# Performance work log

Hardware: AMD Instinct MI355X
Metric: run time of the kernel (lower is better)

## Reference

```python
import jax, jax.numpy as jnp
import numpy as np

NUM_EMBEDDINGS = 1024
EMBEDDING_DIM = 256
COMMITMENT_COST = 0.25


def setup_inputs() -> dict:
    key = jax.random.key(0)
    k1, k2 = jax.random.split(key)
    inputs = jax.random.normal(k1, (32, EMBEDDING_DIM, 32, 32), dtype=jnp.float32)
    # codebook init matches torch: uniform(-1/K, 1/K)
    weight = jax.random.uniform(
        k2, (NUM_EMBEDDINGS, EMBEDDING_DIM), dtype=jnp.float32,
        minval=-1.0 / NUM_EMBEDDINGS, maxval=1.0 / NUM_EMBEDDINGS)
    return {"inputs": inputs, "weight": weight}


def reference(inputs, weight):
    # inputs: [B, C, H, W] with C == EMBEDDING_DIM; weight: [K, D]
    x = jnp.transpose(inputs, (0, 2, 3, 1))            # [B, H, W, D]
    input_shape = x.shape
    flat = x.reshape(-1, EMBEDDING_DIM)                # [N, D]

    distances = (jnp.sum(flat * flat, axis=1, keepdims=True)
                 + jnp.sum(weight * weight, axis=1)
                 - 2.0 * (flat @ weight.T))
    encoding_indices = jnp.argmin(distances, axis=1)   # [N]
    encodings = jax.nn.one_hot(encoding_indices, NUM_EMBEDDINGS, dtype=jnp.float32)  # [N, K]

    # one_hot @ weight == gather; use gather for efficiency (same values)
    quantized = weight[encoding_indices].reshape(input_shape)  # [B, H, W, D]

    e_latent_loss = jnp.mean((jax.lax.stop_gradient(quantized) - x) ** 2)
    q_latent_loss = jnp.mean((quantized - jax.lax.stop_gradient(x)) ** 2)
    loss = q_latent_loss + COMMITMENT_COST * e_latent_loss

    # straight-through estimator
    quantized_st = x + jax.lax.stop_gradient(quantized - x)

    avg_probs = jnp.mean(encodings, axis=0)            # [K]
    perplexity = jnp.exp(-jnp.sum(avg_probs * jnp.log(avg_probs + 1e-10)))

    return (loss,
            jnp.transpose(quantized_st, (0, 3, 1, 2)),  # back to [B, C, H, W]
            perplexity,
            encodings)
```

## Files before the change

kernel.cpp:

```cpp
#include <hip/hip_runtime.h>
#include <hip/hip_bf16.h>

#define HWDIM 1024
#define DDIM 256
#define KCODES 1024
#define NROWS 32768
#define BSTRIDE (DDIM * HWDIM)
#define GUARD 1.5e-4f

typedef __attribute__((ext_vector_type(8))) short short8;
typedef __attribute__((ext_vector_type(4))) float f32x4;
typedef unsigned long long ull;


__device__ __forceinline__ unsigned short f2bf(float v) {
  __hip_bfloat16 b = __float2bfloat16(v);
  return *reinterpret_cast<unsigned short*>(&b);
}
__device__ __forceinline__ float bf2f(unsigned short u) {
  __hip_bfloat16 b;
  *reinterpret_cast<unsigned short*>(&b) = u;
  return __bfloat162float(b);
}
__device__ __forceinline__ ull pk(float d, int k) {
  unsigned ub = __float_as_uint(d);
  ub = (ub & 0x80000000u) ? ~ub : (ub | 0x80000000u);
  return ((ull)ub << 32) | (unsigned)k;
}
__device__ __forceinline__ float keyq(ull key) {
  unsigned ub = (unsigned)(key >> 32);
  unsigned orig = (ub & 0x80000000u) ? (ub & 0x7FFFFFFFu) : ~ub;
  return __uint_as_float(orig);
}

__device__ __forceinline__ float pair128_sq(const float* p, int stride) {
  float a[8];
#pragma unroll
  for (int j = 0; j < 8; ++j) { float v = p[j * stride]; a[j] = __fmul_rn(v, v); }
  for (int i = 8; i < 128; i += 8) {
#pragma unroll
    for (int j = 0; j < 8; ++j) {
      float v = p[(i + j) * stride];
      a[j] = __fadd_rn(a[j], __fmul_rn(v, v));
    }
  }
  float s01 = __fadd_rn(a[0], a[1]), s23 = __fadd_rn(a[2], a[3]);
  float s45 = __fadd_rn(a[4], a[5]), s67 = __fadd_rn(a[6], a[7]);
  return __fadd_rn(__fadd_rn(s01, s23), __fadd_rn(s45, s67));
}

__global__ __launch_bounds__(256) void k_prep(
    const float* __restrict__ w, float* __restrict__ wT, float* __restrict__ ss,
    int* __restrict__ hist, double* __restrict__ loss,
    int* __restrict__ wcount, int* __restrict__ pcount,
    unsigned short* __restrict__ wh8, unsigned short* __restrict__ wl8) {
  __shared__ float tile[64][65];
  const int t = threadIdx.x;
  int g = blockIdx.x * 256 + t;
  {
    int k = g >> 5, oct = g & 31;
    const float* p = w + k * DDIM + oct * 8;
    short8 hv, lv;
#pragma unroll
    for (int j = 0; j < 8; ++j) {
      float v = p[j];
      unsigned short h = f2bf(v);
      unsigned short l = f2bf(__fsub_rn(v, bf2f(h)));
      hv[j] = (short)h; lv[j] = (short)l;
    }
    *(short8*)&wh8[oct * 8192 + k * 8] = hv;
    *(short8*)&wl8[oct * 8192 + k * 8] = lv;
  }
  if (g < KCODES) {
    hist[g] = 0;
    const float* p = w + g * DDIM;
    ss[g] = __fadd_rn(pair128_sq(p, 1), pair128_sq(p + 128, 1));
  }
  if (g == 0) { *loss = 0.0; *wcount = 0; *pcount = 0; }
  if (blockIdx.x < 64) {
    const int k0 = (blockIdx.x & 15) * 64, d0 = (blockIdx.x >> 4) * 64;
    const int c = t & 63, r = t >> 6;
#pragma unroll
    for (int m = 0; m < 16; ++m)
      tile[r + m * 4][c] = w[(k0 + r + m * 4) * DDIM + d0 + c];
    __syncthreads();
#pragma unroll
    for (int m = 0; m < 16; ++m)
      wT[(size_t)(d0 + r + m * 4) * KCODES + k0 + c] = tile[c][r + m * 4];
  }
}

__global__ __launch_bounds__(256) void k_argmfma(
    const float* __restrict__ in,
    const unsigned short* __restrict__ wh8, const unsigned short* __restrict__ wl8,
    const float* __restrict__ ss, unsigned* __restrict__ kkarr,
    int* __restrict__ wlist, int* __restrict__ wcount,
    int* __restrict__ plist, int* __restrict__ pcount) {
  __shared__ __align__(16) unsigned short Ah[32 * 32 * 8];
  __shared__ __align__(16) unsigned short Al[32 * 32 * 8];
  __shared__ __align__(16) float ss_l[1024];
  __shared__ ull best1[32], best2[32], best3[32];

  const int t = threadIdx.x;
  const int n0 = blockIdx.x * 32;
  const int b = n0 >> 10, hw0 = n0 & 1023;

  const int wv = t >> 6, ln = t & 63;
  const int cw = wv * 64;
  const int l15 = ln & 15, quad = ln >> 4;

  {
    const int hw = t & 31, dg = t >> 5;
    const float* xp = in + b * BSTRIDE + hw0 + hw;
#pragma unroll
    for (int dd = 0; dd < 32; dd += 2) {
      int d = dg * 32 + dd;
      float f0 = xp[d * HWDIM], f1 = xp[(d + 1) * HWDIM];
      unsigned short h0 = f2bf(f0);
      unsigned short l0 = f2bf(__fsub_rn(f0, bf2f(h0)));
      unsigned short h1 = f2bf(f1);
      unsigned short l1 = f2bf(__fsub_rn(f1, bf2f(h1)));
      int base = ((d >> 3) * 32 + hw) * 8 + (d & 7);
      *(unsigned*)&Ah[base] = (unsigned)h0 | ((unsigned)h1 << 16);
      *(unsigned*)&Al[base] = (unsigned)l0 | ((unsigned)l1 << 16);
    }
  }
  *(float4*)&ss_l[t * 4] = *(const float4*)&ss[t * 4];
  if (t < 32) { best1[t] = ~0ull; best2[t] = ~0ull; best3[t] = ~0ull; }
  __syncthreads();

  ull rb1[8], rb2[8], rb3[8];
#pragma unroll
  for (int i = 0; i < 8; ++i) { rb1[i] = ~0ull; rb2[i] = ~0ull; rb3[i] = ~0ull; }

  for (int kb = 0; kb < 4; ++kb) {
    const int cb = kb * 256 + cw;
    f32x4 acc[2][4];
#pragma unroll
    for (int rt = 0; rt < 2; ++rt)
#pragma unroll
      for (int ct = 0; ct < 4; ++ct) acc[rt][ct] = (f32x4){0.f, 0.f, 0.f, 0.f};

#pragma unroll
    for (int ki = 0; ki < 8; ++ki) {
      const int obase = ki * 4 + quad;
      short8 ah[2], al[2], bh[4], bl[4];
#pragma unroll
      for (int rt = 0; rt < 2; ++rt) {
        int row = rt * 16 + l15;
        ah[rt] = *(const short8*)&Ah[(obase * 32 + row) * 8];
        al[rt] = *(const short8*)&Al[(obase * 32 + row) * 8];
      }
#pragma unroll
      for (int ct = 0; ct < 4; ++ct) {
        int off = obase * 8192 + (cb + ct * 16 + l15) * 8;
        bh[ct] = *(const short8*)&wh8[off];
        bl[ct] = *(const short8*)&wl8[off];
      }
      __builtin_amdgcn_s_setprio(1);
#pragma unroll
      for (int rt = 0; rt < 2; ++rt)
#pragma unroll
        for (int ct = 0; ct < 4; ++ct) {
          acc[rt][ct] = __builtin_amdgcn_mfma_f32_16x16x32_bf16(ah[rt], bh[ct], acc[rt][ct], 0, 0, 0);
          acc[rt][ct] = __builtin_amdgcn_mfma_f32_16x16x32_bf16(ah[rt], bl[ct], acc[rt][ct], 0, 0, 0);
          acc[rt][ct] = __builtin_amdgcn_mfma_f32_16x16x32_bf16(al[rt], bh[ct], acc[rt][ct], 0, 0, 0);
        }
      __builtin_amdgcn_s_setprio(0);
    }

    float sv[4];
#pragma unroll
    for (int ct = 0; ct < 4; ++ct) sv[ct] = ss_l[cb + ct * 16 + l15];
#pragma unroll
    for (int rt = 0; rt < 2; ++rt)
#pragma unroll
      for (int reg = 0; reg < 4; ++reg) {
        int idx = rt * 4 + reg;
        ull b1 = rb1[idx], b2 = rb2[idx], b3 = rb3[idx];
#pragma unroll
        for (int ct = 0; ct < 4; ++ct) {
          float q = fmaf(-2.f, acc[rt][ct][reg], sv[ct]);
          ull key = pk(q, cb + ct * 16 + l15);
          if (key < b1)      { b3 = b2; b2 = b1; b1 = key; }
          else if (key < b2) { b3 = b2; b2 = key; }
          else if (key < b3) { b3 = key; }
        }
        rb1[idx] = b1; rb2[idx] = b2; rb3[idx] = b3;
      }
  }

#pragma unroll
  for (int rt = 0; rt < 2; ++rt)
#pragma unroll
    for (int reg = 0; reg < 4; ++reg)
      atomicMin(&best1[rt * 16 + quad * 4 + reg], rb1[rt * 4 + reg]);
  __syncthreads();
#pragma unroll
  for (int rt = 0; rt < 2; ++rt)
#pragma unroll
    for (int reg = 0; reg < 4; ++reg) {
      int row = rt * 16 + quad * 4 + reg;
      int idx = rt * 4 + reg;
      ull sub = (rb1[idx] == best1[row]) ? rb2[idx] : rb1[idx];
      atomicMin(&best2[row], sub);
    }
  __syncthreads();
#pragma unroll
  for (int rt = 0; rt < 2; ++rt)
#pragma unroll
    for (int reg = 0; reg < 4; ++reg) {
      int row = rt * 16 + quad * 4 + reg;
      int idx = rt * 4 + reg;
      ull b1 = best1[row], b2 = best2[row];
      ull c = (rb1[idx] != b1 && rb1[idx] != b2) ? rb1[idx]
            : ((rb2[idx] != b1 && rb2[idx] != b2) ? rb2[idx] : rb3[idx]);
      atomicMin(&best3[row], c);
    }
  __syncthreads();
  if (t < 32) {
    ull k1 = best1[t];
    kkarr[n0 + t] = (unsigned)(k1 & 0xFFFFFFFFull);
    float q1 = keyq(k1);
    if (!(keyq(best2[t]) - q1 > GUARD)) {
      if (keyq(best3[t]) - q1 > GUARD) {
        int p = atomicAdd(pcount, 1);
        plist[p] = (n0 + t) | ((int)(best2[t] & 0xFFFFFFFFull) << 16);
      } else {
        int p = atomicAdd(wcount, 1);
        wlist[p] = n0 + t;
      }
    }
  }
}

__global__ __launch_bounds__(256) void k_fallback(
    const float* __restrict__ in, const float* __restrict__ w,
    const float* __restrict__ wT, const float* __restrict__ ss,
    const int* __restrict__ wlist, const int* __restrict__ wcount,
    const int* __restrict__ plist, const int* __restrict__ pcount,
    unsigned* __restrict__ kkarr) {
  __shared__ float xrow[256];
  __shared__ float rsh;
  __shared__ ull bmin;
  __shared__ ull pkeys[2];
  const int t = threadIdx.x;

  const int pc = *pcount;
  for (int i = blockIdx.x; i < pc; i += gridDim.x) {
    const int pe = plist[i];
    const int n = pe & 0xFFFF;
    const unsigned k2 = ((unsigned)pe) >> 16;
    const unsigned k1 = kkarr[n];
    const int b = n >> 10, hw = n & 1023;
    xrow[t] = in[b * BSTRIDE + t * HWDIM + hw];
    __syncthreads();
    if (t == 0) rsh = __fadd_rn(pair128_sq(xrow, 1), pair128_sq(xrow + 128, 1));
    __syncthreads();
    if (t < 2) {
      unsigned k = t ? k2 : k1;
      const float* wr = w + (size_t)k * DDIM;
      float m = 0.f;
      for (int d = 0; d < 256; ++d) m = fmaf(xrow[d], wr[d], m);
      float dist = fmaf(-2.f, m, __fadd_rn(rsh, ss[k]));
      pkeys[t] = pk(dist, (int)k);
    }
    __syncthreads();
    if (t == 0) {
      ull kmin = pkeys[0] < pkeys[1] ? pkeys[0] : pkeys[1];
      kkarr[n] = (unsigned)(kmin & 0xFFFFFFFFull);
    }
    __syncthreads();
  }

  const int cnt = *wcount;
  for (int i = blockIdx.x; i < cnt; i += gridDim.x) {
    const int n = wlist[i];
    const int b = n >> 10, hw = n & 1023;
    xrow[t] = in[b * BSTRIDE + t * HWDIM + hw];
    if (t == 0) bmin = ~0ull;
    __syncthreads();
    if (t == 0) rsh = __fadd_rn(pair128_sq(xrow, 1), pair128_sq(xrow + 128, 1));
    __syncthreads();
    float m[4] = {0.f, 0.f, 0.f, 0.f};
    for (int d = 0; d < 256; ++d) {
      float xv = xrow[d];
      const float* wd = wT + (size_t)d * KCODES + t;
      m[0] = fmaf(xv, wd[0], m[0]);
      m[1] = fmaf(xv, wd[256], m[1]);
      m[2] = fmaf(xv, wd[512], m[2]);
      m[3] = fmaf(xv, wd[768], m[3]);
    }
    ull lb = ~0ull;
#pragma unroll
    for (int j = 0; j < 4; ++j) {
      int k = t + j * 256;
      float dist = fmaf(-2.f, m[j], __fadd_rn(rsh, ss[k]));
      ull key = pk(dist, k);
      if (key < lb) lb = key;
    }
    atomicMin(&bmin, lb);
    __syncthreads();
    if (t == 0) kkarr[n] = (unsigned)(bmin & 0xFFFFFFFFull);
    __syncthreads();
  }
}

__global__ __launch_bounds__(256) void k_quantenc(
    const float* __restrict__ in, const float* __restrict__ w,
    const unsigned* __restrict__ kkarr, int* __restrict__ hist,
    float* __restrict__ enc, float* __restrict__ outq, double* __restrict__ loss) {
  __shared__ float wrow[64][65];
  __shared__ unsigned kk[64];
  __shared__ double red[256];

  const int t = threadIdx.x;
  const int q = blockIdx.x & 3;
  const int n0 = (blockIdx.x >> 2) * 64;
  const int dc = q * 64;
  const int c0 = q * 256;
  const int b = n0 >> 10, hw0 = n0 & 1023;

  if (t < 64) kk[t] = kkarr[n0 + t];
  __syncthreads();

  if (q == 0 && t < 64) atomicAdd(&hist[kk[t]], 1);

#pragma unroll 4
  for (int m = 0; m < 32; ++m) {
    int u = m * 256 + t;
    int r = u >> 7, c2 = u & 127;
    int cbase = c0 + c2 * 2;
    unsigned kr = kk[r];
    float2 v;
    v.x = (cbase == (int)kr) ? 1.0f : 0.0f;
    v.y = (cbase + 1 == (int)kr) ? 1.0f : 0.0f;
    *(float2*)&enc[(size_t)(n0 + r) * 1024 + cbase] = v;
  }

#pragma unroll
  for (int m = 0; m < 16; ++m) {
    int u = t + m * 256;
    int r = u >> 6, dd = u & 63;
    wrow[r][dd] = w[kk[r] * DDIM + dc + dd];
  }
  __syncthreads();

  const float* inb = in + b * BSTRIDE + hw0;
  float* outb = outq + b * BSTRIDE + hw0;
  const int hwl = t & 63, dl = t >> 6;
  double lsum = 0.0;
#pragma unroll
  for (int dd = 0; dd < 64; dd += 4) {
    int d = dc + dd + dl;
    float x = inb[d * HWDIM + hwl];
    float wv = wrow[hwl][dd + dl];
    float diff = __fsub_rn(wv, x);
    outb[d * HWDIM + hwl] = __fadd_rn(x, diff);
    lsum += (double)diff * (double)diff;
  }
  red[t] = lsum;
  __syncthreads();
  for (int s = 128; s > 0; s >>= 1) {
    if (t < s) red[t] += red[t + s];
    __syncthreads();
  }
  if (t == 0) atomicAdd(loss, red[0]);
}

__global__ void k_final(const int* __restrict__ hist, const double* __restrict__ loss,
                        float* __restrict__ out) {
  __shared__ double red[256];
  int t = threadIdx.x;
  double s = 0.0;
  for (int i = t; i < KCODES; i += 256) {
    double p = (double)hist[i] * (1.0 / 32768.0);
    s += p * log(p + 1e-10);
  }
  red[t] = s;
  __syncthreads();
  for (int st = 128; st > 0; st >>= 1) {
    if (t < st) red[t] += red[t + st];
    __syncthreads();
  }
  if (t == 0) {
    out[8388609] = (float)exp(-red[0]);
    double m = *loss / 8388608.0;
    out[0] = (float)(1.25 * m);
  }
}

extern "C" void kernel_launch(void* const* d_in, const int* in_sizes, int n_in,
                              void* d_out, int out_size, void* d_ws, size_t ws_size,
                              hipStream_t stream) {
  const float* in = (const float*)d_in[0];
  const float* w  = (const float*)d_in[1];
  float* out = (float*)d_out;

  char* wsb = (char*)d_ws;
  float*    wT     = (float*)   (wsb + 0);
  float*    ssp    = (float*)   (wsb + 1048576);
  unsigned* kkarr  = (unsigned*)(wsb + 1052672);
  int*      wlist  = (int*)     (wsb + 1183744);
  int*      hist   = (int*)     (wsb + 1314816);
  int*      plist  = (int*)     (wsb + 1318912);
  double*   loss   = (double*)  (wsb + 1449984);
  int*      wcount = (int*)     (wsb + 1449992);
  int*      pcount = (int*)     (wsb + 1449996);

  char* ob = (char*)d_out + 33554448;
  unsigned short* wh8 = (unsigned short*)(ob + 0);
  unsigned short* wl8 = (unsigned short*)(ob + 524288);
  float* encp = out + 8388610;

  k_prep<<<dim3(128), dim3(256), 0, stream>>>(w, wT, ssp, hist, loss, wcount, pcount, wh8, wl8);
  k_argmfma<<<dim3(1024), dim3(256), 0, stream>>>(in, wh8, wl8, ssp, kkarr,
                                                  wlist, wcount, plist, pcount);
  k_fallback<<<dim3(1024), dim3(256), 0, stream>>>(in, w, wT, ssp, wlist, wcount,
                                                   plist, pcount, kkarr);
  k_quantenc<<<dim3(2048), dim3(256), 0, stream>>>(in, w, kkarr, hist, encp,
                                                   out + 1, loss);
  k_final<<<dim3(1), dim3(256), 0, stream>>>(hist, loss, out);
}
```

Before: 355.7 us.

## Double rows per block in argmin MFMA kernel and pad LDS layout

Each block of the argmin MFMA kernel now handles 64 input rows instead of 32, so every codebook fragment loaded from global memory feeds twice as many MFMAs and the grid halves to 512 blocks. The A-operand LDS layout gets a padded stride to reduce bank conflicts, input loads use nontemporal hints, and the third-best tracker is shrunk to a 32-bit distance key to save registers. Launch bounds of one block per CU with 16 accumulator tiles raise register pressure and may reduce occupancy or cause spills.

```diff
diff --git a/kernel.cpp b/kernel.cpp
--- a/kernel.cpp
+++ b/kernel.cpp
@@ -7,6 +7,7 @@
 #define NROWS 32768
 #define BSTRIDE (DDIM * HWDIM)
 #define GUARD 1.5e-4f
+#define APAD 520
 
 typedef __attribute__((ext_vector_type(8))) short short8;
 typedef __attribute__((ext_vector_type(4))) float f32x4;
@@ -29,6 +30,10 @@
 }
 __device__ __forceinline__ float keyq(ull key) {
   unsigned ub = (unsigned)(key >> 32);
+  unsigned orig = (ub & 0x80000000u) ? (ub & 0x7FFFFFFFu) : ~ub;
+  return __uint_as_float(orig);
+}
+__device__ __forceinline__ float keyq32(unsigned ub) {
   unsigned orig = (ub & 0x80000000u) ? (ub & 0x7FFFFFFFu) : ~ub;
   return __uint_as_float(orig);
 }
@@ -90,19 +95,20 @@
   }
 }
 
-__global__ __launch_bounds__(256) void k_argmfma(
+__global__ __launch_bounds__(256, 1) void k_argmfma(
     const float* __restrict__ in,
     const unsigned short* __restrict__ wh8, const unsigned short* __restrict__ wl8,
     const float* __restrict__ ss, unsigned* __restrict__ kkarr,
     int* __restrict__ wlist, int* __restrict__ wcount,
     int* __restrict__ plist, int* __restrict__ pcount) {
-  __shared__ __align__(16) unsigned short Ah[32 * 32 * 8];
-  __shared__ __align__(16) unsigned short Al[32 * 32 * 8];
+  __shared__ __align__(16) unsigned short Ah[32 * APAD];
+  __shared__ __align__(16) unsigned short Al[32 * APAD];
   __shared__ __align__(16) float ss_l[1024];
-  __shared__ ull best1[32], best2[32], best3[32];
+  __shared__ ull best1[64], best2[64];
+  __shared__ unsigned best3[64];
 
   const int t = threadIdx.x;
-  const int n0 = blockIdx.x * 32;
+  const int n0 = blockIdx.x * 64;
   const int b = n0 >> 10, hw0 = n0 & 1023;
 
   const int wv = t >> 6, ln = t & 63;
@@ -110,46 +116,48 @@
   const int l15 = ln & 15, quad = ln >> 4;
 
   {
-    const int hw = t & 31, dg = t >> 5;
+    const int hw = t & 63, dg = t >> 6;
     const float* xp = in + b * BSTRIDE + hw0 + hw;
 #pragma unroll
-    for (int dd = 0; dd < 32; dd += 2) {
-      int d = dg * 32 + dd;
-      float f0 = xp[d * HWDIM], f1 = xp[(d + 1) * HWDIM];
+    for (int dd = 0; dd < 64; dd += 2) {
+      int d = dg * 64 + dd;
+      float f0 = __builtin_nontemporal_load(&xp[d * HWDIM]);
+      float f1 = __builtin_nontemporal_load(&xp[(d + 1) * HWDIM]);
       unsigned short h0 = f2bf(f0);
       unsigned short l0 = f2bf(__fsub_rn(f0, bf2f(h0)));
       unsigned short h1 = f2bf(f1);
       unsigned short l1 = f2bf(__fsub_rn(f1, bf2f(h1)));
-      int base = ((d >> 3) * 32 + hw) * 8 + (d & 7);
+      int base = (d >> 3) * APAD + hw * 8 + (d & 7);
       *(unsigned*)&Ah[base] = (unsigned)h0 | ((unsigned)h1 << 16);
       *(unsigned*)&Al[base] = (unsigned)l0 | ((unsigned)l1 << 16);
     }
   }
   *(float4*)&ss_l[t * 4] = *(const float4*)&ss[t * 4];
-  if (t < 32) { best1[t] = ~0ull; best2[t] = ~0ull; best3[t] = ~0ull; }
-  __syncthreads();
-
-  ull rb1[8], rb2[8], rb3[8];
-#pragma unroll
-  for (int i = 0; i < 8; ++i) { rb1[i] = ~0ull; rb2[i] = ~0ull; rb3[i] = ~0ull; }
+  if (t < 64) { best1[t] = ~0ull; best2[t] = ~0ull; best3[t] = 0xFFFFFFFFu; }
+  __syncthreads();
+
+  ull rb1[16], rb2[16];
+  unsigned rb3[16];
+#pragma unroll
+  for (int i = 0; i < 16; ++i) { rb1[i] = ~0ull; rb2[i] = ~0ull; rb3[i] = 0xFFFFFFFFu; }
 
   for (int kb = 0; kb < 4; ++kb) {
     const int cb = kb * 256 + cw;
-    f32x4 acc[2][4];
-#pragma unroll
-    for (int rt = 0; rt < 2; ++rt)
+    f32x4 acc[4][4];
+#pragma unroll
+    for (int rt = 0; rt < 4; ++rt)
 #pragma unroll
       for (int ct = 0; ct < 4; ++ct) acc[rt][ct] = (f32x4){0.f, 0.f, 0.f, 0.f};
 
 #pragma unroll
     for (int ki = 0; ki < 8; ++ki) {
       const int obase = ki * 4 + quad;
-      short8 ah[2], al[2], bh[4], bl[4];
-#pragma unroll
-      for (int rt = 0; rt < 2; ++rt) {
+      short8 ah[4], al[4], bh[4], bl[4];
+#pragma unroll
+      for (int rt = 0; rt < 4; ++rt) {
         int row = rt * 16 + l15;
-        ah[rt] = *(const short8*)&Ah[(obase * 32 + row) * 8];
-        al[rt] = *(const short8*)&Al[(obase * 32 + row) * 8];
+        ah[rt] = *(const short8*)&Ah[obase * APAD + row * 8];
+        al[rt] = *(const short8*)&Al[obase * APAD + row * 8];
       }
 #pragma unroll
       for (int ct = 0; ct < 4; ++ct) {
@@ -159,7 +167,7 @@
       }
       __builtin_amdgcn_s_setprio(1);
 #pragma unroll
-      for (int rt = 0; rt < 2; ++rt)
+      for (int rt = 0; rt < 4; ++rt)
 #pragma unroll
         for (int ct = 0; ct < 4; ++ct) {
           acc[rt][ct] = __builtin_amdgcn_mfma_f32_16x16x32_bf16(ah[rt], bh[ct], acc[rt][ct], 0, 0, 0);
@@ -173,31 +181,33 @@
 #pragma unroll
     for (int ct = 0; ct < 4; ++ct) sv[ct] = ss_l[cb + ct * 16 + l15];
 #pragma unroll
-    for (int rt = 0; rt < 2; ++rt)
+    for (int rt = 0; rt < 4; ++rt)
 #pragma unroll
       for (int reg = 0; reg < 4; ++reg) {
         int idx = rt * 4 + reg;
-        ull b1 = rb1[idx], b2 = rb2[idx], b3 = rb3[idx];
+        ull b1 = rb1[idx], b2 = rb2[idx];
+        unsigned b3 = rb3[idx];
 #pragma unroll
         for (int ct = 0; ct < 4; ++ct) {
           float q = fmaf(-2.f, acc[rt][ct][reg], sv[ct]);
           ull key = pk(q, cb + ct * 16 + l15);
-          if (key < b1)      { b3 = b2; b2 = b1; b1 = key; }
-          else if (key < b2) { b3 = b2; b2 = key; }
-          else if (key < b3) { b3 = key; }
+          unsigned k32 = (unsigned)(key >> 32);
+          if (key < b1)      { b3 = (unsigned)(b2 >> 32); b2 = b1; b1 = key; }
+          else if (key < b2) { b3 = (unsigned)(b2 >> 32); b2 = key; }
+          else if (k32 < b3) { b3 = k32; }
         }
         rb1[idx] = b1; rb2[idx] = b2; rb3[idx] = b3;
       }
   }
 
 #pragma unroll
-  for (int rt = 0; rt < 2; ++rt)
+  for (int rt = 0; rt < 4; ++rt)
 #pragma unroll
     for (int reg = 0; reg < 4; ++reg)
       atomicMin(&best1[rt * 16 + quad * 4 + reg], rb1[rt * 4 + reg]);
   __syncthreads();
 #pragma unroll
-  for (int rt = 0; rt < 2; ++rt)
+  for (int rt = 0; rt < 4; ++rt)
 #pragma unroll
     for (int reg = 0; reg < 4; ++reg) {
       int row = rt * 16 + quad * 4 + reg;
@@ -207,23 +217,24 @@
     }
   __syncthreads();
 #pragma unroll
-  for (int rt = 0; rt < 2; ++rt)
+  for (int rt = 0; rt < 4; ++rt)
 #pragma unroll
     for (int reg = 0; reg < 4; ++reg) {
       int row = rt * 16 + quad * 4 + reg;
       int idx = rt * 4 + reg;
       ull b1 = best1[row], b2 = best2[row];
-      ull c = (rb1[idx] != b1 && rb1[idx] != b2) ? rb1[idx]
-            : ((rb2[idx] != b1 && rb2[idx] != b2) ? rb2[idx] : rb3[idx]);
+      unsigned c = (rb1[idx] != b1 && rb1[idx] != b2) ? (unsigned)(rb1[idx] >> 32)
+                 : ((rb2[idx] != b1 && rb2[idx] != b2) ? (unsigned)(rb2[idx] >> 32)
+                                                       : rb3[idx]);
       atomicMin(&best3[row], c);
     }
   __syncthreads();
-  if (t < 32) {
+  if (t < 64) {
     ull k1 = best1[t];
     kkarr[n0 + t] = (unsigned)(k1 & 0xFFFFFFFFull);
     float q1 = keyq(k1);
     if (!(keyq(best2[t]) - q1 > GUARD)) {
-      if (keyq(best3[t]) - q1 > GUARD) {
+      if (keyq32(best3[t]) - q1 > GUARD) {
         int p = atomicAdd(pcount, 1);
         plist[p] = (n0 + t) | ((int)(best2[t] & 0xFFFFFFFFull) << 16);
       } else {
@@ -414,8 +425,8 @@
   float* encp = out + 8388610;
 
   k_prep<<<dim3(128), dim3(256), 0, stream>>>(w, wT, ssp, hist, loss, wcount, pcount, wh8, wl8);
-  k_argmfma<<<dim3(1024), dim3(256), 0, stream>>>(in, wh8, wl8, ssp, kkarr,
-                                                  wlist, wcount, plist, pcount);
+  k_argmfma<<<dim3(512), dim3(256), 0, stream>>>(in, wh8, wl8, ssp, kkarr,
+                                                 wlist, wcount, plist, pcount);
   k_fallback<<<dim3(1024), dim3(256), 0, stream>>>(in, w, wT, ssp, wlist, wcount,
                                                    plist, pcount, kkarr);
   k_quantenc<<<dim3(2048), dim3(256), 0, stream>>>(in, w, kkarr, hist, encp,
```

Result: faster. 348.3 us (-2.1%).

## Shrink argmin kernel register footprint to raise occupancy in MFMA distance search

Applied to the files above, without the earlier changes.

Halves each wave's column tile (two 16-column tiles instead of four, eight codebook passes instead of four), stores the third-best candidate as a 32-bit value instead of a 64-bit key, and adds a launch_bounds occupancy hint of 4. The goal is to cut VGPR use so more waves fit per CU and hide codebook load latency. Input loads become nontemporal. In exchange each wave issues more loop iterations, with less reuse of A fragments per B load, and the third-best now keeps only the distance bits, which is enough for the guard test.

```diff
diff --git a/kernel.cpp b/kernel.cpp
--- a/kernel.cpp
+++ b/kernel.cpp
@@ -29,6 +29,10 @@
 }
 __device__ __forceinline__ float keyq(ull key) {
   unsigned ub = (unsigned)(key >> 32);
+  unsigned orig = (ub & 0x80000000u) ? (ub & 0x7FFFFFFFu) : ~ub;
+  return __uint_as_float(orig);
+}
+__device__ __forceinline__ float keyq32(unsigned ub) {
   unsigned orig = (ub & 0x80000000u) ? (ub & 0x7FFFFFFFu) : ~ub;
   return __uint_as_float(orig);
 }
@@ -90,7 +94,7 @@
   }
 }
 
-__global__ __launch_bounds__(256) void k_argmfma(
+__global__ __launch_bounds__(256, 4) void k_argmfma(
     const float* __restrict__ in,
     const unsigned short* __restrict__ wh8, const unsigned short* __restrict__ wl8,
     const float* __restrict__ ss, unsigned* __restrict__ kkarr,
@@ -99,14 +103,15 @@
   __shared__ __align__(16) unsigned short Ah[32 * 32 * 8];
   __shared__ __align__(16) unsigned short Al[32 * 32 * 8];
   __shared__ __align__(16) float ss_l[1024];
-  __shared__ ull best1[32], best2[32], best3[32];
+  __shared__ ull best1[32], best2[32];
+  __shared__ unsigned best3[32];
 
   const int t = threadIdx.x;
   const int n0 = blockIdx.x * 32;
   const int b = n0 >> 10, hw0 = n0 & 1023;
 
   const int wv = t >> 6, ln = t & 63;
-  const int cw = wv * 64;
+  const int cw = wv * 32;
   const int l15 = ln & 15, quad = ln >> 4;
 
   {
@@ -115,7 +120,8 @@
 #pragma unroll
     for (int dd = 0; dd < 32; dd += 2) {
       int d = dg * 32 + dd;
-      float f0 = xp[d * HWDIM], f1 = xp[(d + 1) * HWDIM];
+      float f0 = __builtin_nontemporal_load(&xp[d * HWDIM]);
+      float f1 = __builtin_nontemporal_load(&xp[(d + 1) * HWDIM]);
       unsigned short h0 = f2bf(f0);
       unsigned short l0 = f2bf(__fsub_rn(f0, bf2f(h0)));
       unsigned short h1 = f2bf(f1);
@@ -126,25 +132,26 @@
     }
   }
   *(float4*)&ss_l[t * 4] = *(const float4*)&ss[t * 4];
-  if (t < 32) { best1[t] = ~0ull; best2[t] = ~0ull; best3[t] = ~0ull; }
-  __syncthreads();
-
-  ull rb1[8], rb2[8], rb3[8];
-#pragma unroll
-  for (int i = 0; i < 8; ++i) { rb1[i] = ~0ull; rb2[i] = ~0ull; rb3[i] = ~0ull; }
-
-  for (int kb = 0; kb < 4; ++kb) {
-    const int cb = kb * 256 + cw;
-    f32x4 acc[2][4];
+  if (t < 32) { best1[t] = ~0ull; best2[t] = ~0ull; best3[t] = 0xFFFFFFFFu; }
+  __syncthreads();
+
+  ull rb1[8], rb2[8];
+  unsigned rb3[8];
+#pragma unroll
+  for (int i = 0; i < 8; ++i) { rb1[i] = ~0ull; rb2[i] = ~0ull; rb3[i] = 0xFFFFFFFFu; }
+
+  for (int kb = 0; kb < 8; ++kb) {
+    const int cb = kb * 128 + cw;
+    f32x4 acc[2][2];
 #pragma unroll
     for (int rt = 0; rt < 2; ++rt)
 #pragma unroll
-      for (int ct = 0; ct < 4; ++ct) acc[rt][ct] = (f32x4){0.f, 0.f, 0.f, 0.f};
+      for (int ct = 0; ct < 2; ++ct) acc[rt][ct] = (f32x4){0.f, 0.f, 0.f, 0.f};
 
 #pragma unroll
     for (int ki = 0; ki < 8; ++ki) {
       const int obase = ki * 4 + quad;
-      short8 ah[2], al[2], bh[4], bl[4];
+      short8 ah[2], al[2], bh[2], bl[2];
 #pragma unroll
       for (int rt = 0; rt < 2; ++rt) {
         int row = rt * 16 + l15;
@@ -152,7 +159,7 @@
         al[rt] = *(const short8*)&Al[(obase * 32 + row) * 8];
       }
 #pragma unroll
-      for (int ct = 0; ct < 4; ++ct) {
+      for (int ct = 0; ct < 2; ++ct) {
         int off = obase * 8192 + (cb + ct * 16 + l15) * 8;
         bh[ct] = *(const short8*)&wh8[off];
         bl[ct] = *(const short8*)&wl8[off];
@@ -161,7 +168,7 @@
 #pragma unroll
       for (int rt = 0; rt < 2; ++rt)
 #pragma unroll
-        for (int ct = 0; ct < 4; ++ct) {
+        for (int ct = 0; ct < 2; ++ct) {
           acc[rt][ct] = __builtin_amdgcn_mfma_f32_16x16x32_bf16(ah[rt], bh[ct], acc[rt][ct], 0, 0, 0);
           acc[rt][ct] = __builtin_amdgcn_mfma_f32_16x16x32_bf16(ah[rt], bl[ct], acc[rt][ct], 0, 0, 0);
           acc[rt][ct] = __builtin_amdgcn_mfma_f32_16x16x32_bf16(al[rt], bh[ct], acc[rt][ct], 0, 0, 0);
@@ -169,22 +176,24 @@
       __builtin_amdgcn_s_setprio(0);
     }
 
-    float sv[4];
-#pragma unroll
-    for (int ct = 0; ct < 4; ++ct) sv[ct] = ss_l[cb + ct * 16 + l15];
+    float sv[2];
+#pragma unroll
+    for (int ct = 0; ct < 2; ++ct) sv[ct] = ss_l[cb + ct * 16 + l15];
 #pragma unroll
     for (int rt = 0; rt < 2; ++rt)
 #pragma unroll
       for (int reg = 0; reg < 4; ++reg) {
         int idx = rt * 4 + reg;
-        ull b1 = rb1[idx], b2 = rb2[idx], b3 = rb3[idx];
-#pragma unroll
-        for (int ct = 0; ct < 4; ++ct) {
+        ull b1 = rb1[idx], b2 = rb2[idx];
+        unsigned b3 = rb3[idx];
+#pragma unroll
+        for (int ct = 0; ct < 2; ++ct) {
           float q = fmaf(-2.f, acc[rt][ct][reg], sv[ct]);
           ull key = pk(q, cb + ct * 16 + l15);
-          if (key < b1)      { b3 = b2; b2 = b1; b1 = key; }
-          else if (key < b2) { b3 = b2; b2 = key; }
-          else if (key < b3) { b3 = key; }
+          unsigned k32 = (unsigned)(key >> 32);
+          if (key < b1)      { b3 = (unsigned)(b2 >> 32); b2 = b1; b1 = key; }
+          else if (key < b2) { b3 = (unsigned)(b2 >> 32); b2 = key; }
+          else if (k32 < b3) { b3 = k32; }
         }
         rb1[idx] = b1; rb2[idx] = b2; rb3[idx] = b3;
       }
@@ -213,8 +222,9 @@
       int row = rt * 16 + quad * 4 + reg;
       int idx = rt * 4 + reg;
       ull b1 = best1[row], b2 = best2[row];
-      ull c = (rb1[idx] != b1 && rb1[idx] != b2) ? rb1[idx]
-            : ((rb2[idx] != b1 && rb2[idx] != b2) ? rb2[idx] : rb3[idx]);
+      unsigned c = (rb1[idx] != b1 && rb1[idx] != b2) ? (unsigned)(rb1[idx] >> 32)
+                 : ((rb2[idx] != b1 && rb2[idx] != b2) ? (unsigned)(rb2[idx] >> 32)
+                                                       : rb3[idx]);
       atomicMin(&best3[row], c);
     }
   __syncthreads();
@@ -223,7 +233,7 @@
     kkarr[n0 + t] = (unsigned)(k1 & 0xFFFFFFFFull);
     float q1 = keyq(k1);
     if (!(keyq(best2[t]) - q1 > GUARD)) {
-      if (keyq(best3[t]) - q1 > GUARD) {
+      if (keyq32(best3[t]) - q1 > GUARD) {
         int p = atomicAdd(pcount, 1);
         plist[p] = (n0 + t) | ((int)(best2[t] & 0xFFFFFFFFull) << 16);
       } else {
```

Measured after the change: 465.5 us. 30.9% more time.
